# Optimization experiments

Hardware: AMD Instinct MI355X
Metric: run time of the kernel (lower is better)

Reference implementation:

```python
import jax, jax.numpy as jnp
import numpy as np

ENC_VTH = 0.999      # ENCODER_REGULAR_VTH
CDECAY = 0.5         # NEURON_CDECAY
VDECAY = 0.75        # NEURON_VDECAY
VTH = 0.5            # NEURON_VTH
WIN = 0.5            # SPIKE_PSEUDO_GRAD_WINDOW
T = 5                # spike_ts

# --- pseudo-gradient spike functions ---
@jax.custom_vjp
def enc_spike(v):
    return (v > ENC_VTH).astype(v.dtype)
def _enc_fwd(v):
    return enc_spike(v), None
def _enc_bwd(_, g):
    return (g,)  # straight-through
enc_spike.defvjp(_enc_fwd, _enc_bwd)

@jax.custom_vjp
def rect_spike(v):
    return (v > VTH).astype(v.dtype)
def _rect_fwd(v):
    return rect_spike(v), v
def _rect_bwd(v, g):
    return (g * (jnp.abs(v - VTH) < WIN).astype(g.dtype),)
rect_spike.defvjp(_rect_fwd, _rect_bwd)


def setup_inputs() -> dict:
    key = jax.random.key(0)
    ks = jax.random.split(key, 8)
    B, obs_dim, en_pop, act_dim, de_pop = 8192, 128, 10, 8, 10
    H1, H2 = 256, 256
    N = obs_dim * en_pop           # 1280
    O = act_dim * de_pop           # 80
    obs = jax.random.normal(ks[0], (B, obs_dim), jnp.float32)
    # encoder mean: linspace over mean_range per population, std constant 0.15
    mean_row = jnp.linspace(-3.0, 3.0, en_pop, dtype=jnp.float32)
    enc_mean = jnp.broadcast_to(mean_row, (1, obs_dim, en_pop)).astype(jnp.float32)
    enc_std = jnp.full((1, obs_dim, en_pop), 0.15, jnp.float32)
    W1 = jax.random.normal(ks[1], (H1, N), jnp.float32) / np.sqrt(N)
    b1 = jnp.zeros((H1,), jnp.float32)
    W2 = jax.random.normal(ks[2], (H2, H1), jnp.float32) / np.sqrt(H1)
    b2 = jnp.zeros((H2,), jnp.float32)
    Wo = jax.random.normal(ks[3], (O, H2), jnp.float32) / np.sqrt(H2)
    bo = jnp.zeros((O,), jnp.float32)
    dec_w = jax.random.normal(ks[4], (act_dim, de_pop), jnp.float32) / np.sqrt(de_pop)
    dec_b = jnp.zeros((act_dim,), jnp.float32)
    log_std = jnp.full((act_dim,), -0.001, jnp.float32)
    return {"obs": obs, "enc_mean": enc_mean, "enc_std": enc_std,
            "W1": W1, "b1": b1, "W2": W2, "b2": b2, "Wo": Wo, "bo": bo,
            "dec_w": dec_w, "dec_b": dec_b, "log_std": log_std}


def reference(obs, enc_mean, enc_std, W1, b1, W2, b2, Wo, bo, dec_w, dec_b, log_std):
    B = obs.shape[0]
    # --- population encoder: gaussian receptive fields -> regular spike train ---
    pop_act = jnp.exp(-0.5 * (obs[:, :, None] - enc_mean) ** 2 / enc_std ** 2)
    pop_act = pop_act.reshape(B, -1)  # [B, obs_dim*en_pop]

    def enc_step(volt, _):
        volt = volt + pop_act
        s = enc_spike(volt)
        return volt - s * ENC_VTH, s
    _, spikes = jax.lax.scan(enc_step, jnp.zeros_like(pop_act), None, length=T)  # [T, B, N]

    # --- LIF neuron model ---
    def lif(x, W, b, c, v, s):
        c = c * CDECAY + x @ W.T + b
        v = v * VDECAY * (1.0 - s) + c
        s = rect_spike(v)
        return c, v, s

    H1, H2, O = W1.shape[0], W2.shape[0], Wo.shape[0]
    z = lambda n: jnp.zeros((B, n), dtype=obs.dtype)
    carry0 = ((z(H1), z(H1), z(H1)), (z(H2), z(H2), z(H2)), (z(O), z(O), z(O)), z(O))

    def snn_step(carry, x):
        (c1, v1, s1), (c2, v2, s2), (co, vo, so), acc = carry
        c1, v1, s1 = lif(x, W1, b1, c1, v1, s1)
        c2, v2, s2 = lif(s1, W2, b2, c2, v2, s2)
        co, vo, so = lif(s2, Wo, bo, co, vo, so)
        return ((c1, v1, s1), (c2, v2, s2), (co, vo, so), acc + so), None

    (_, _, _, acc), _ = jax.lax.scan(snn_step, carry0, spikes)
    out_pop_act = acc / T  # [B, act_dim*de_pop]

    # --- grouped Conv1d(kernel=de_pop, groups=act_dim) decoder + ELU ---
    act_dim, de_pop = dec_w.shape
    mu = jax.nn.elu(jnp.einsum('bap,ap->ba', out_pop_act.reshape(B, act_dim, de_pop), dec_w) + dec_b)
    std = jnp.exp(log_std)
    return mu, std
```

## Files before the change

kernel.cpp:

```cpp
#include <hip/hip_runtime.h>

typedef unsigned char  u8;
typedef unsigned short u16;
typedef unsigned int   u32;
typedef unsigned long long u64;
typedef __attribute__((ext_vector_type(8))) short bf16x8;
typedef __attribute__((ext_vector_type(4))) float f32x4;

#define NOBS 128
#define NN   1280
#define NH   256
#define NO   80
#define TT   5
#define RR   16
#define NTHR 512
#define BP1  88
#define BP2  20

#define W1TOT   983040
#define W2S_OFF 983040
#define WOS_OFF 1179648
#define WS_TOTAL 1277952

#define PREP_BLOCKS 208

#define VMW2()  asm volatile("s_waitcnt vmcnt(2)" ::: "memory")
#define VMW0()  asm volatile("s_waitcnt vmcnt(0)" ::: "memory")
#define FENCE() asm volatile("" ::: "memory")

__device__ __forceinline__ float bf2f(u16 u) {
  union { u32 i; float f; } x; x.i = ((u32)u) << 16; return x.f;
}
__device__ __forceinline__ u16 f2bf(float f) {
  union { float f; u32 i; } x; x.f = f;
  u32 i = x.i + 0x7FFFu + ((x.i >> 16) & 1u);
  return (u16)(i >> 16);
}

__device__ __forceinline__ float exp_cr(float arg) {
  double xa = (double)arg;
  double nd = __builtin_rint(xa * 1.4426950408889634074);
  double r  = fma(nd, -6.93147180369123816490e-01, xa);
  r         = fma(nd, -1.90821492927058770002e-10, r);
  double p = 2.50521083854417187751e-08;
  p = fma(p, r, 2.75573192239858906526e-07);
  p = fma(p, r, 2.75573192239858906526e-06);
  p = fma(p, r, 2.48015873015873015873e-05);
  p = fma(p, r, 1.98412698412698412698e-04);
  p = fma(p, r, 1.38888888888888888889e-03);
  p = fma(p, r, 8.33333333333333333333e-03);
  p = fma(p, r, 4.16666666666666666667e-02);
  p = fma(p, r, 1.66666666666666666667e-01);
  p = fma(p, r, 0.5);
  p = fma(p, r, 1.0);
  p = fma(p, r, 1.0);
  int n = (int)nd;
  union { u64 u; double d; } s;
  s.u = ((u64)(u32)(n + 1023)) << 52;
  return (n < -150) ? 0.f : (float)(s.d * p);
}

__global__ __launch_bounds__(256) void prep_w(
    const float* __restrict__ W1, const float* __restrict__ W2,
    const float* __restrict__ Wo, u16* __restrict__ ws)
{
  const int T = blockIdx.x * 256 + threadIdx.x;
  const float* src;
  int dstb, selstep;
  bool pad = false;
  if (T < 40960) {
    int kcks = T >> 10, r = T & 1023;
    int kc = kcks >> 1, ks = kcks & 1, j = r >> 2, kgrp = r & 3;
    int kk0 = (kgrp ^ ((j >> 1) & 3)) << 3;
    src = W1 + j * 1280 + kc * 64 + ks * 32 + kk0;
    dstb = kc * 49152 + ks * 24576 + j * 32 + kgrp * 8;
    selstep = 8192;
  } else if (T < 49152) {
    int T2 = T - 40960;
    int kcks = T2 >> 10, r = T2 & 1023;
    int kc = kcks >> 1, ks = kcks & 1, j = r >> 2, kgrp = r & 3;
    int kk0 = (kgrp ^ ((j >> 1) & 3)) << 3;
    src = W2 + j * 256 + kc * 64 + ks * 32 + kk0;
    dstb = W2S_OFF + kc * 49152 + ks * 24576 + j * 32 + kgrp * 8;
    selstep = 8192;
  } else {
    int T3 = T - 49152;
    int kcks = T3 >> 9, r = T3 & 511;
    int kc = kcks >> 1, ks = kcks & 1, j = r >> 2, kgrp = r & 3;
    int kk0 = (kgrp ^ ((j >> 1) & 3)) << 3;
    src = Wo + j * 256 + kc * 64 + ks * 32 + kk0;
    dstb = WOS_OFF + kc * 24576 + ks * 12288 + j * 32 + kgrp * 8;
    selstep = 4096;
    pad = (j >= NO);
  }
  float w[8];
  if (!pad) {
    float4 w0 = *(const float4*)src;
    float4 w1 = *(const float4*)(src + 4);
    w[0] = w0.x; w[1] = w0.y; w[2] = w0.z; w[3] = w0.w;
    w[4] = w1.x; w[5] = w1.y; w[6] = w1.z; w[7] = w1.w;
  } else {
    #pragma unroll
    for (int e = 0; e < 8; ++e) w[e] = 0.f;
  }
  union { u16 u[8]; uint4 q; } hi, mid, lo;
  #pragma unroll
  for (int e = 0; e < 8; ++e) {
    u16 h = f2bf(w[e]);
    float r1 = __fsub_rn(w[e], bf2f(h));
    u16 m = f2bf(r1);
    float r2 = __fsub_rn(r1, bf2f(m));
    hi.u[e] = h; mid.u[e] = m; lo.u[e] = f2bf(r2);
  }
  *(uint4*)(ws + dstb)               = hi.q;
  *(uint4*)(ws + dstb + selstep)     = mid.q;
  *(uint4*)(ws + dstb + 2 * selstep) = lo.q;
}

__device__ __forceinline__ void dma2(const u16* __restrict__ lane_src, u16* dst) {
  __builtin_amdgcn_global_load_lds((const u32*)lane_src, (u32*)dst, 16, 0, 0);
  __builtin_amdgcn_global_load_lds((const u32*)(lane_src + 512),
                                   (u32*)(dst + 512), 16, 0, 0);
}

__device__ __forceinline__ void gemm_wp(
    const u16* lbits, int bpitch,
    const u16* __restrict__ wsbase, int nkc, int selblk,
    u16* mybuf, const u64* __restrict__ lut,
    int wv, int lane, f32x4 acc[2][TT])
{
  const int m16 = lane & 15, q = lane >> 4;
  const int swz = (q ^ ((m16 >> 1) & 3)) * 8;
  const int lro0 = m16 * 32 + swz;
  const int lro1 = lro0 + 512;
  const int sh = q * 8;
  const int nst = nkc * 6;
  const u16* lsrc = wsbase + wv * 1024 + lane * 8;

  dma2(lsrc, mybuf);
  dma2(lsrc + selblk, mybuf + 1024);
  const u16* nsrc = lsrc + 2 * selblk;
  FENCE();
  VMW2();
  bf16x8 cur0 = *(const bf16x8*)(mybuf + lro0);
  bf16x8 cur1 = *(const bf16x8*)(mybuf + lro1);
  FENCE();

  int st = 0;
  for (int kcks = 0; kcks < nkc * 2; ++kcks) {
    const int kc = kcks >> 1, ks = kcks & 1;
    bf16x8 afr[TT];
    #pragma unroll
    for (int t = 0; t < TT; ++t) {
      u32 bwv = *(const u32*)(lbits + (t * RR + m16) * bpitch + kc * 4 + ks * 2);
      u32 b = (bwv >> sh) & 0xFFu;
      union { u64 d[2]; bf16x8 v; } x;
      x.d[0] = lut[b & 15u];
      x.d[1] = lut[b >> 4];
      afr[t] = x.v;
    }
    #pragma unroll
    for (int sel = 0; sel < 3; ++sel, ++st) {
      if (st + 2 < nst) {
        dma2(nsrc, mybuf + ((sel + 2) % 3) * 1024);
        nsrc += selblk;
      }
      FENCE();
      #pragma unroll
      for (int t = 0; t < TT; ++t)
        acc[0][t] = __builtin_amdgcn_mfma_f32_16x16x32_bf16(afr[t], cur0, acc[0][t], 0, 0, 0);
      #pragma unroll
      for (int t = 0; t < TT; ++t)
        acc[1][t] = __builtin_amdgcn_mfma_f32_16x16x32_bf16(afr[t], cur1, acc[1][t], 0, 0, 0);
      if (st + 1 < nst) {
        if (st + 2 < nst) { VMW2(); } else { VMW0(); }
        const u16* nb = mybuf + ((sel + 1) % 3) * 1024;
        cur0 = *(const bf16x8*)(nb + lro0);
        cur1 = *(const bf16x8*)(nb + lro1);
      }
      FENCE();
    }
  }
}

__device__ __forceinline__ void recur_spikes2(
    f32x4 acc[2][TT], const float* __restrict__ bias,
    int lane, int wv, u16* sbits, int spitch)
{
  const int q = lane >> 4, m16 = lane & 15;
  #pragma unroll
  for (int i = 0; i < 2; ++i) {
    int ct = wv * 2 + i;
    int j = ct * 16 + m16;
    float bj = bias[j];
    #pragma unroll
    for (int rg = 0; rg < 4; ++rg) {
      float c = 0.f, v = 0.f, sprev = 0.f;
      #pragma unroll
      for (int t = 0; t < TT; ++t) {
        float u = acc[i][t][rg];
        c = __fadd_rn(__fadd_rn(__fmul_rn(c, 0.5f), u), bj);
        float vd = __fmul_rn(v, 0.75f);
        v = __fadd_rn((sprev > 0.5f) ? 0.f : vd, c);
        bool sp = v > 0.5f;
        u64 mask = __ballot(sp);
        if (m16 == 0) {
          int row = q * 4 + rg;
          sbits[(t * RR + row) * spitch + ct] = (u16)(mask >> (q * 16));
        }
        sprev = sp ? 1.f : 0.f;
      }
    }
  }
}

__global__ __launch_bounds__(NTHR, 4) void snn_main(
    const float* __restrict__ obs, const float* __restrict__ enc_mean,
    const float* __restrict__ enc_std,
    const float* __restrict__ b1, const float* __restrict__ b2, const float* __restrict__ bo,
    const float* __restrict__ dec_w, const float* __restrict__ dec_b, const float* __restrict__ log_std,
    const u16* __restrict__ wsW, float* __restrict__ out, int Btot)
{
  __shared__ __align__(16) u16 smem[37440];
  u16* bufs = smem;
  u16* encb = smem + 24576;
  u16* s1b  = encb + 7040;
  u16* s2b  = s1b + 1600;
  float* soacc = (float*)(s2b + 1600);
  u64* lutp = (u64*)(smem + 37376);

  const int tid  = threadIdx.x;
  const int lane = tid & 63;
  const int wv   = tid >> 6;
  const int r0   = blockIdx.x * RR;
  u16* mybuf = bufs + wv * 3072;

  if (tid < 16) {
    u32 lo32 = (((tid & 3u) * 0x8001u) & 0x10001u) * 0x3F80u;
    u32 hi32 = ((((tid >> 2) & 3u) * 0x8001u) & 0x10001u) * 0x3F80u;
    lutp[tid] = (u64)lo32 | ((u64)hi32 << 32);
  }

  for (int h = tid; h < RR * 160; h += NTHR) {
    int r = h / 160, rem = h - r * 160;
    int w = rem >> 1, hi = rem & 1;
    const float* obsrow = obs + (r0 + r) * NOBS;
    u32 bits[TT] = {0, 0, 0, 0, 0};
    #pragma unroll
    for (int e = 0; e < 8; ++e) {
      int k = w * 16 + hi * 8 + e;
      int f = k / 10;
      float x  = obsrow[f];
      float m  = enc_mean[k];
      float sd = enc_std[k];
      float d  = __fsub_rn(x, m);
      float arg = __fdiv_rn(__fmul_rn(-0.5f, __fmul_rn(d, d)), __fmul_rn(sd, sd));
      float a = exp_cr(arg);
      float v = 0.f;
      #pragma unroll
      for (int t = 0; t < TT; ++t) {
        v = __fadd_rn(v, a);
        if (v > 0.999f) { bits[t] |= (1u << e); v = __fsub_rn(v, 0.999f); }
      }
    }
    u8* eb = (u8*)encb;
    #pragma unroll
    for (int t = 0; t < TT; ++t)
      eb[((t * RR + r) * BP1 + w) * 2 + hi] = (u8)bits[t];
  }
  __syncthreads();

  f32x4 acc[2][TT];
  const f32x4 zero4 = {0.f, 0.f, 0.f, 0.f};
#define ZERO_ACC() { _Pragma("unroll") for (int i = 0; i < 2; ++i) \
                     _Pragma("unroll") for (int t = 0; t < TT; ++t) acc[i][t] = zero4; }

  ZERO_ACC();
  gemm_wp(encb, BP1, wsW, 20, 8192, mybuf, lutp, wv, lane, acc);
  recur_spikes2(acc, b1, lane, wv, s1b, BP2);
  __syncthreads();

  ZERO_ACC();
  gemm_wp(s1b, BP2, wsW + W2S_OFF, 4, 8192, mybuf, lutp, wv, lane, acc);
  recur_spikes2(acc, b2, lane, wv, s2b, BP2);
  __syncthreads();

  if (wv < 3) {
    ZERO_ACC();
    gemm_wp(s2b, BP2, wsW + WOS_OFF, 4, 4096, mybuf, lutp, wv, lane, acc);
    const int q = lane >> 4, m16 = lane & 15;
    #pragma unroll
    for (int i = 0; i < 2; ++i) {
      int j = (wv * 2 + i) * 16 + m16;
      bool valid = j < NO;
      float bj = valid ? bo[j] : 0.f;
      #pragma unroll
      for (int rg = 0; rg < 4; ++rg) {
        float c = 0.f, v = 0.f, sprev = 0.f;
        int cnt = 0;
        #pragma unroll
        for (int t = 0; t < TT; ++t) {
          float u = acc[i][t][rg];
          c = __fadd_rn(__fadd_rn(__fmul_rn(c, 0.5f), u), bj);
          float vd = __fmul_rn(v, 0.75f);
          v = __fadd_rn((sprev > 0.5f) ? 0.f : vd, c);
          bool sp = v > 0.5f;
          cnt += sp ? 1 : 0;
          sprev = sp ? 1.f : 0.f;
        }
        if (valid) soacc[(q * 4 + rg) * NO + j] = __fdiv_rn((float)cnt, 5.0f);
      }
    }
  }
  __syncthreads();

  if (tid < RR * 8) {
    int r = tid >> 3, a = tid & 7;
    float s = 0.f;
    const float* so = soacc + r * NO + a * 10;
    #pragma unroll
    for (int p = 0; p < 10; ++p)
      s = __fadd_rn(s, __fmul_rn(so[p], dec_w[a * 10 + p]));
    s = __fadd_rn(s, dec_b[a]);
    float mu = (s > 0.f) ? s : expm1f(s);
    out[(r0 + r) * 8 + a] = mu;
  }
  if (blockIdx.x == 0 && tid < 8) {
    out[Btot * 8 + tid] = expf(log_std[tid]);
  }
}

extern "C" void kernel_launch(void* const* d_in, const int* in_sizes, int n_in,
                              void* d_out, int out_size, void* d_ws, size_t ws_size,
                              hipStream_t stream) {
  const float* obs      = (const float*)d_in[0];
  const float* enc_mean = (const float*)d_in[1];
  const float* enc_std  = (const float*)d_in[2];
  const float* W1       = (const float*)d_in[3];
  const float* b1       = (const float*)d_in[4];
  const float* W2       = (const float*)d_in[5];
  const float* b2       = (const float*)d_in[6];
  const float* Wo       = (const float*)d_in[7];
  const float* bo       = (const float*)d_in[8];
  const float* dec_w    = (const float*)d_in[9];
  const float* dec_b    = (const float*)d_in[10];
  const float* log_std  = (const float*)d_in[11];
  u16*   ws  = (u16*)d_ws;
  float* out = (float*)d_out;
  int B = in_sizes[0] / NOBS;

  hipLaunchKernelGGL(prep_w, dim3(PREP_BLOCKS), dim3(256), 0, stream,
                     W1, W2, Wo, ws);
  hipLaunchKernelGGL(snn_main, dim3(B / RR), dim3(NTHR), 0, stream,
                     obs, enc_mean, enc_std, b1, b2, bo, dec_w, dec_b, log_std,
                     ws, out, B);
}
```

Measured before the change: 167.9 us.

## Load weight fragments directly into registers instead of staging through LDS

Replaces the per-wave triple-buffered global_load_lds DMA pipeline with direct global-to-register loads of the pre-swizzled weight fragments, using a two-deep register double buffer. This removes the LDS staging buffers, cutting shared memory from about 75KB to about 26KB per block, which could allow more blocks per CU and removes LDS read traffic and manual waitcnt fences. The risk is that the compiler's waitcnt placement may expose global-load latency in front of the MFMAs, since the software prefetch is now only two steps ahead.

```diff
diff --git a/kernel.cpp b/kernel.cpp
--- a/kernel.cpp
+++ b/kernel.cpp
@@ -23,10 +23,6 @@
 #define WS_TOTAL 1277952
 
 #define PREP_BLOCKS 208
-
-#define VMW2()  asm volatile("s_waitcnt vmcnt(2)" ::: "memory")
-#define VMW0()  asm volatile("s_waitcnt vmcnt(0)" ::: "memory")
-#define FENCE() asm volatile("" ::: "memory")
 
 __device__ __forceinline__ float bf2f(u16 u) {
   union { u32 i; float f; } x; x.i = ((u32)u) << 16; return x.f;
@@ -117,68 +113,62 @@
   *(uint4*)(ws + dstb + 2 * selstep) = lo.q;
 }
 
-__device__ __forceinline__ void dma2(const u16* __restrict__ lane_src, u16* dst) {
-  __builtin_amdgcn_global_load_lds((const u32*)lane_src, (u32*)dst, 16, 0, 0);
-  __builtin_amdgcn_global_load_lds((const u32*)(lane_src + 512),
-                                   (u32*)(dst + 512), 16, 0, 0);
-}
-
-__device__ __forceinline__ void gemm_wp(
+__device__ __forceinline__ void build_afr(
+    const u16* lbits, int bpitch, int kc, int ks, int m16, int sh,
+    const u64* __restrict__ lut, bf16x8 afr[TT])
+{
+  #pragma unroll
+  for (int t = 0; t < TT; ++t) {
+    u32 bwv = *(const u32*)(lbits + (t * RR + m16) * bpitch + kc * 4 + ks * 2);
+    u32 b = (bwv >> sh) & 0xFFu;
+    union { u64 d[2]; bf16x8 v; } x;
+    x.d[0] = lut[b & 15u];
+    x.d[1] = lut[b >> 4];
+    afr[t] = x.v;
+  }
+}
+
+__device__ __forceinline__ void gemm_reg(
     const u16* lbits, int bpitch,
     const u16* __restrict__ wsbase, int nkc, int selblk,
-    u16* mybuf, const u64* __restrict__ lut,
-    int wv, int lane, f32x4 acc[2][TT])
+    const u64* __restrict__ lut, int wv, int lane, f32x4 acc[2][TT])
 {
   const int m16 = lane & 15, q = lane >> 4;
   const int swz = (q ^ ((m16 >> 1) & 3)) * 8;
-  const int lro0 = m16 * 32 + swz;
-  const int lro1 = lro0 + 512;
   const int sh = q * 8;
   const int nst = nkc * 6;
-  const u16* lsrc = wsbase + wv * 1024 + lane * 8;
-
-  dma2(lsrc, mybuf);
-  dma2(lsrc + selblk, mybuf + 1024);
-  const u16* nsrc = lsrc + 2 * selblk;
-  FENCE();
-  VMW2();
-  bf16x8 cur0 = *(const bf16x8*)(mybuf + lro0);
-  bf16x8 cur1 = *(const bf16x8*)(mybuf + lro1);
-  FENCE();
-
+  const u16* lb = wsbase + wv * 1024 + m16 * 32 + swz;
+
+  bf16x8 e0a = *(const bf16x8*)(lb);
+  bf16x8 e0b = *(const bf16x8*)(lb + 512);
+  bf16x8 o1a = *(const bf16x8*)(lb + selblk);
+  bf16x8 o1b = *(const bf16x8*)(lb + selblk + 512);
+  const u16* nsrc = lb + 2 * selblk;
   int st = 0;
-  for (int kcks = 0; kcks < nkc * 2; ++kcks) {
-    const int kc = kcks >> 1, ks = kcks & 1;
-    bf16x8 afr[TT];
-    #pragma unroll
-    for (int t = 0; t < TT; ++t) {
-      u32 bwv = *(const u32*)(lbits + (t * RR + m16) * bpitch + kc * 4 + ks * 2);
-      u32 b = (bwv >> sh) & 0xFFu;
-      union { u64 d[2]; bf16x8 v; } x;
-      x.d[0] = lut[b & 15u];
-      x.d[1] = lut[b >> 4];
-      afr[t] = x.v;
-    }
-    #pragma unroll
-    for (int sel = 0; sel < 3; ++sel, ++st) {
-      if (st + 2 < nst) {
-        dma2(nsrc, mybuf + ((sel + 2) % 3) * 1024);
-        nsrc += selblk;
+
+  for (int kc = 0; kc < nkc; ++kc) {
+    #pragma unroll
+    for (int ks = 0; ks < 2; ++ks) {
+      bf16x8 afr[TT];
+      build_afr(lbits, bpitch, kc, ks, m16, sh, lut, afr);
+      #pragma unroll
+      for (int sel = 0; sel < 3; ++sel, ++st) {
+        const bool even = (((3 * ks + sel) & 1) == 0);
+        const bf16x8 ca = even ? e0a : o1a;
+        const bf16x8 cb = even ? e0b : o1b;
+        #pragma unroll
+        for (int t = 0; t < TT; ++t)
+          acc[0][t] = __builtin_amdgcn_mfma_f32_16x16x32_bf16(afr[t], ca, acc[0][t], 0, 0, 0);
+        #pragma unroll
+        for (int t = 0; t < TT; ++t)
+          acc[1][t] = __builtin_amdgcn_mfma_f32_16x16x32_bf16(afr[t], cb, acc[1][t], 0, 0, 0);
+        if (st + 2 < nst) {
+          bf16x8 na = *(const bf16x8*)(nsrc);
+          bf16x8 nb = *(const bf16x8*)(nsrc + 512);
+          if (even) { e0a = na; e0b = nb; } else { o1a = na; o1b = nb; }
+          nsrc += selblk;
+        }
       }
-      FENCE();
-      #pragma unroll
-      for (int t = 0; t < TT; ++t)
-        acc[0][t] = __builtin_amdgcn_mfma_f32_16x16x32_bf16(afr[t], cur0, acc[0][t], 0, 0, 0);
-      #pragma unroll
-      for (int t = 0; t < TT; ++t)
-        acc[1][t] = __builtin_amdgcn_mfma_f32_16x16x32_bf16(afr[t], cur1, acc[1][t], 0, 0, 0);
-      if (st + 1 < nst) {
-        if (st + 2 < nst) { VMW2(); } else { VMW0(); }
-        const u16* nb = mybuf + ((sel + 1) % 3) * 1024;
-        cur0 = *(const bf16x8*)(nb + lro0);
-        cur1 = *(const bf16x8*)(nb + lro1);
-      }
-      FENCE();
     }
   }
 }
@@ -221,19 +211,17 @@
     const float* __restrict__ dec_w, const float* __restrict__ dec_b, const float* __restrict__ log_std,
     const u16* __restrict__ wsW, float* __restrict__ out, int Btot)
 {
-  __shared__ __align__(16) u16 smem[37440];
-  u16* bufs = smem;
-  u16* encb = smem + 24576;
-  u16* s1b  = encb + 7040;
-  u16* s2b  = s1b + 1600;
-  float* soacc = (float*)(s2b + 1600);
-  u64* lutp = (u64*)(smem + 37376);
+  __shared__ __align__(16) u16 smem[12864];
+  u16* encb = smem;
+  u16* s1b  = smem + 7040;
+  u16* s2b  = smem + 8640;
+  float* soacc = (float*)(smem + 10240);
+  u64* lutp = (u64*)(smem + 12800);
 
   const int tid  = threadIdx.x;
   const int lane = tid & 63;
   const int wv   = tid >> 6;
   const int r0   = blockIdx.x * RR;
-  u16* mybuf = bufs + wv * 3072;
 
   if (tid < 16) {
     u32 lo32 = (((tid & 3u) * 0x8001u) & 0x10001u) * 0x3F80u;
@@ -276,18 +264,18 @@
                      _Pragma("unroll") for (int t = 0; t < TT; ++t) acc[i][t] = zero4; }
 
   ZERO_ACC();
-  gemm_wp(encb, BP1, wsW, 20, 8192, mybuf, lutp, wv, lane, acc);
+  gemm_reg(encb, BP1, wsW, 20, 8192, lutp, wv, lane, acc);
   recur_spikes2(acc, b1, lane, wv, s1b, BP2);
   __syncthreads();
 
   ZERO_ACC();
-  gemm_wp(s1b, BP2, wsW + W2S_OFF, 4, 8192, mybuf, lutp, wv, lane, acc);
+  gemm_reg(s1b, BP2, wsW + W2S_OFF, 4, 8192, lutp, wv, lane, acc);
   recur_spikes2(acc, b2, lane, wv, s2b, BP2);
   __syncthreads();
 
   if (wv < 3) {
     ZERO_ACC();
-    gemm_wp(s2b, BP2, wsW + WOS_OFF, 4, 4096, mybuf, lutp, wv, lane, acc);
+    gemm_reg(s2b, BP2, wsW + WOS_OFF, 4, 4096, lutp, wv, lane, acc);
     const int q = lane >> 4, m16 = lane & 15;
     #pragma unroll
     for (int i = 0; i < 2; ++i) {
```

Result: faster. 157.1 us (-6.4%).
